# Kernel tuning notes

Measured on AMD Instinct MI355X. Metric: run time of the kernel, lower is better.

## Reference

```python
import jax, jax.numpy as jnp
import numpy as np

VOCAB, EMB, HID, TEMP = 10000, 256, 512, 0.5
EPS = 1e-20


def _lstm(x_seq, h0, c0, Wih, Whh, b):
    # x_seq: [T, B, E]; PyTorch gate order i, f, g, o
    def step(carry, x):
        h, c = carry
        gates = x @ Wih + h @ Whh + b
        i, f, g, o = jnp.split(gates, 4, axis=-1)
        c = jax.nn.sigmoid(f) * c + jax.nn.sigmoid(i) * jnp.tanh(g)
        h = jax.nn.sigmoid(o) * jnp.tanh(c)
        return (h, c), h
    (hT, cT), hs = jax.lax.scan(step, (h0, c0), x_seq)
    return hs, hT, cT


def setup_inputs() -> dict:
    key = jax.random.key(0)
    ks = jax.random.split(key, 16)
    B, T = 32, 128
    s = 0.02
    input_ids = jax.random.randint(ks[0], (B, T), 0, VOCAB, dtype=jnp.int32)
    mask = jax.random.randint(ks[1], (B, T), 0, 2, dtype=jnp.int32)
    U = jax.random.uniform(ks[2], (T, B, VOCAB), dtype=jnp.float32)
    gumbel_noise = -jnp.log(-jnp.log(U + EPS) + EPS)
    return {
        'input_ids': input_ids,
        'my_attention_mask': mask,
        'enc_embed': s * jax.random.normal(ks[3], (VOCAB, EMB), jnp.float32),
        'enc_Wih': s * jax.random.normal(ks[4], (EMB, 4 * HID), jnp.float32),
        'enc_Whh': s * jax.random.normal(ks[5], (HID, 4 * HID), jnp.float32),
        'enc_b': jnp.zeros((4 * HID,), jnp.float32),
        'dec_embed': s * jax.random.normal(ks[6], (VOCAB, EMB), jnp.float32),
        'dec_Wih': s * jax.random.normal(ks[7], (EMB, 4 * HID), jnp.float32),
        'dec_Whh': s * jax.random.normal(ks[8], (HID, 4 * HID), jnp.float32),
        'dec_b': jnp.zeros((4 * HID,), jnp.float32),
        'fc_W': s * jax.random.normal(ks[9], (HID, VOCAB), jnp.float32),
        'fc_b': jnp.zeros((VOCAB,), jnp.float32),
        'rand_init': jax.random.uniform(ks[10], (T, B, VOCAB), dtype=jnp.float32),
        'gumbel_noise': gumbel_noise,
    }


def reference(input_ids, my_attention_mask, enc_embed, enc_Wih, enc_Whh, enc_b,
              dec_embed, dec_Wih, dec_Whh, dec_b, fc_W, fc_b,
              rand_init, gumbel_noise):
    B, T = input_ids.shape
    mask = my_attention_mask                      # [B, T]
    tokens = input_ids.T                          # [T, B] (torch.t of view)

    h0 = jnp.zeros((B, HID), jnp.float32)
    # Encoder over full sequence
    _, hT, cT = _lstm(enc_embed[tokens], h0, h0, enc_Wih, enc_Whh, enc_b)
    # Decoder: teacher-forced on tokens[0:T-1] -> outputs for steps t=1..T-1
    hs, _, _ = _lstm(dec_embed[tokens[:-1]], hT, cT, dec_Wih, dec_Whh, dec_b)
    logits = hs @ fc_W + fc_b                     # [T-1, B, V]

    # Mask-driven compaction: outputs[sum(mask[j,:t]), j] = logits[t-1, j] where mask[j,t]==1
    excl = jnp.cumsum(mask, axis=1) - mask        # exclusive prefix sum [B, T]
    pos = excl[:, 1:]                             # [B, T-1]
    valid = mask[:, 1:] > 0
    pos_use = jnp.where(valid, pos, T)            # out-of-range -> dropped
    jj = jnp.broadcast_to(jnp.arange(B)[:, None], pos_use.shape)
    outputs = rand_init.at[pos_use, jj].set(jnp.swapaxes(logits, 0, 1), mode='drop')  # [T, B, V]

    # Hard gumbel-softmax with straight-through
    y = jax.nn.softmax((outputs + gumbel_noise) / TEMP, axis=-1)
    y_hard = jax.nn.one_hot(jnp.argmax(y, axis=-1), VOCAB, dtype=y.dtype)
    gs = jax.lax.stop_gradient(y_hard - y) + y    # [T, B, V]

    # Re-expand: masked positions take compacted gumbel rows, unmasked take token one-hots
    gathered = gs[excl, jnp.arange(B)[:, None]]   # [B, T, V]
    tok_oh = jax.nn.one_hot(input_ids, VOCAB, dtype=jnp.float32)
    onehots = jnp.where((mask > 0)[..., None], gathered, tok_oh)  # [B, T, V]
    return onehots.reshape(-1, VOCAB)             # dense form of the sparse inputs_embeds
```

## Files before the change

### kernel.cpp

```cpp
#include <hip/hip_runtime.h>
#include <hip/hip_bf16.h>
#include <math.h>

#define BB 32
#define TT 128
#define TD 127
#define EMB 256
#define HID 512
#define G4 2048
#define NV 10000
#define NB 64
#define NWK 192
#define GRID_UBER (NB + NWK)
#define UPB 8
#define NT_STEPS (TT + TD)

#define NJOB_DEC 512
#define NJOB_TR  313
#define NJOB_WN  20
#define NJOB_RM  4096
#define NJOBS (NJOB_DEC + NJOB_TR + NJOB_WN + NJOB_RM)

typedef __attribute__((ext_vector_type(8))) short short8v;
typedef __attribute__((ext_vector_type(4))) float f32x4;

__device__ __forceinline__ unsigned short bf16_rne(float x){
    unsigned int u = __float_as_uint(x);
    u += 0x7fffu + ((u >> 16) & 1u);
    return (unsigned short)(u >> 16);
}
__device__ __forceinline__ float bf16f(unsigned short h){
    return __uint_as_float(((unsigned int)h) << 16);
}

__global__ __launch_bounds__(256) void gemm_x(const int* __restrict__ ids,
        const float* __restrict__ embed, const float* __restrict__ W,
        const float* __restrict__ bias, float* __restrict__ X, int M)
{
    __shared__ float As[16][128];
    __shared__ float Bs[16][128];
    __shared__ int toks[128];
    const int tid = threadIdx.x;
    const int m0 = blockIdx.y * 128, n0 = blockIdx.x * 128;
    if (tid < 128) {
        int mr = m0 + tid, tk = 0;
        if (mr < M) { int t = mr >> 5, b = mr & 31; tk = ids[b*TT + t]; }
        toks[tid] = tk;
    }
    __syncthreads();
    float acc[8][8] = {};
    const int ty = tid >> 4, tx = tid & 15;
    for (int kt = 0; kt < EMB; kt += 16) {
        #pragma unroll
        for (int i = 0; i < 2; i++) {
            int idx = tid*2 + i;
            int row = idx >> 2, k4 = (idx & 3)*4;
            float4 a = *(const float4*)&embed[(size_t)toks[row]*EMB + kt + k4];
            As[k4+0][row] = a.x; As[k4+1][row] = a.y; As[k4+2][row] = a.z; As[k4+3][row] = a.w;
        }
        #pragma unroll
        for (int i = 0; i < 2; i++) {
            int idx = tid*2 + i;
            int kr = idx >> 5, c4 = (idx & 31)*4;
            *(float4*)&Bs[kr][c4] = *(const float4*)&W[(size_t)(kt+kr)*G4 + n0 + c4];
        }
        __syncthreads();
        #pragma unroll
        for (int k = 0; k < 16; k++) {
            float a8[8], b8[8];
            #pragma unroll
            for (int i = 0; i < 8; i++) a8[i] = As[k][ty*8+i];
            #pragma unroll
            for (int j = 0; j < 8; j++) b8[j] = Bs[k][tx*8+j];
            #pragma unroll
            for (int i = 0; i < 8; i++) {
                #pragma unroll
                for (int j = 0; j < 8; j++)
                    acc[i][j] = fmaf(a8[i], b8[j], acc[i][j]);
            }
        }
        __syncthreads();
    }
    #pragma unroll
    for (int i = 0; i < 8; i++) {
        int mr = m0 + ty*8 + i;
        if (mr < M) {
            int tt = mr >> 5, bb2 = mr & 31;
            #pragma unroll
            for (int j = 0; j < 8; j++) {
                int nc = n0 + tx*8 + j;
                X[((size_t)tt*G4 + nc)*BB + bb2] = acc[i][j] + bias[nc];
            }
        }
    }
}

__global__ __launch_bounds__(512) void lstm_persist(
        const float* __restrict__ Xenc, float* __restrict__ Xdec,
        const float* __restrict__ Whh_e, const float* __restrict__ Whh_d,
        unsigned int* __restrict__ h_pk,
        float* __restrict__ hs,
        int* __restrict__ flags,
        int* __restrict__ decdone,
        const int* __restrict__ ids, const float* __restrict__ dEmb,
        const float* __restrict__ dWih, const float* __restrict__ dB,
        const float* __restrict__ fcW, float* __restrict__ fcWt,
        const float* __restrict__ fcb, const int* __restrict__ mask,
        const float* __restrict__ gum, float* __restrict__ Mr,
        unsigned int* __restrict__ scal)
{
    __shared__ float smem[11392];
    const int tid = threadIdx.x;
    const int bid = blockIdx.x;

    if (bid >= NB) {
        const int wid = bid - NB;
        for (int job = wid; job < NJOBS; job += NWK) {
            if (job < NJOB_DEC) {
                const int my = job >> 4, nx = job & 15;
                const int m0 = my*128, n0 = nx*128;
                const int M = TD*BB;
                float* As = smem;
                float* Bs = smem + 2048;
                int* toks = (int*)(smem + 4096);
                if (tid < 128) {
                    int mr = m0 + tid, tk = 0;
                    if (mr < M) { int t = mr >> 5, b2 = mr & 31; tk = ids[b2*TT + t]; }
                    toks[tid] = tk;
                }
                __syncthreads();
                float acc[4][8] = {};
                const int ty = tid >> 4, tx = tid & 15;
                for (int kt = 0; kt < EMB; kt += 16) {
                    {
                        int row = tid >> 2, k4 = (tid & 3)*4;
                        float4 a = *(const float4*)&dEmb[(size_t)toks[row]*EMB + kt + k4];
                        As[(k4+0)*128+row] = a.x; As[(k4+1)*128+row] = a.y;
                        As[(k4+2)*128+row] = a.z; As[(k4+3)*128+row] = a.w;
                    }
                    {
                        int kr = tid >> 5, c4 = (tid & 31)*4;
                        *(float4*)&Bs[kr*128 + c4] =
                            *(const float4*)&dWih[(size_t)(kt+kr)*G4 + n0 + c4];
                    }
                    __syncthreads();
                    #pragma unroll
                    for (int k = 0; k < 16; k++) {
                        float a4[4], b8[8];
                        #pragma unroll
                        for (int i = 0; i < 4; i++) a4[i] = As[k*128 + ty*4+i];
                        #pragma unroll
                        for (int j = 0; j < 8; j++) b8[j] = Bs[k*128 + tx*8+j];
                        #pragma unroll
                        for (int i = 0; i < 4; i++) {
                            #pragma unroll
                            for (int j = 0; j < 8; j++)
                                acc[i][j] = fmaf(a4[i], b8[j], acc[i][j]);
                        }
                    }
                    __syncthreads();
                }
                #pragma unroll
                for (int i = 0; i < 4; i++) {
                    int mr = m0 + ty*4 + i;
                    if (mr < M) {
                        int t = mr >> 5, b2 = mr & 31;
                        #pragma unroll
                        for (int j = 0; j < 8; j++) {
                            int nc = n0 + tx*8 + j;
                            Xdec[((size_t)t*G4 + nc)*BB + b2] = acc[i][j] + dB[nc];
                        }
                    }
                }
                __syncthreads();
                if (tid == 0)
                    __hip_atomic_fetch_add(decdone, 1,
                        __ATOMIC_RELEASE, __HIP_MEMORY_SCOPE_AGENT);
            } else if (job < NJOB_DEC + NJOB_TR) {
                const int v0 = (job - NJOB_DEC)*32;
                float* tile = smem;
                for (int k0 = 0; k0 < HID; k0 += 16) {
                    {
                        int kk = tid >> 5, vv = tid & 31;
                        int v = v0 + vv;
                        tile[kk*33 + vv] = (v < NV) ? fcW[(size_t)(k0+kk)*NV + v] : 0.f;
                    }
                    __syncthreads();
                    {
                        int vy = tid >> 4, kx = tid & 15;
                        int v = v0 + vy;
                        if (v < NV) fcWt[(size_t)v*HID + k0 + kx] = tile[kx*33 + vy];
                    }
                    __syncthreads();
                }
            } else if (job < NJOB_DEC + NJOB_TR + NJOB_WN) {
                int v = (job - NJOB_DEC - NJOB_TR)*512 + tid;
                if (v < NV) {
                    float s = 0.f;
                    for (int k = 0; k < HID; k++) {
                        float x = fcW[(size_t)k*NV + v]; s = fmaf(x, x, s);
                    }
                    atomicMax(&scal[0], __float_as_uint(s));
                    atomicMax(&scal[1], __float_as_uint(fabsf(fcb[v])));
                }
            } else {
                const int row = job - NJOB_DEC - NJOB_TR - NJOB_WN;
                const int b = row >> 7, t = row & 127;
                const int mrow = mask[row];
                if (t != 0 && mrow != 0) {
                    int* wk = (int*)&smem[520];
                    int mi = (tid < TT) ? mask[b*TT + tid] : 0;
                    unsigned long long bal = __ballot(tid < t && mi != 0);
                    if ((tid & 63) == 0) wk[tid >> 6] = __popcll(bal);
                    __syncthreads();
                    int k = wk[0] + wk[1];
                    __syncthreads();
                    const float* g = gum + ((size_t)k*BB + b)*NV;
                    float m = -1e30f;
                    for (int v = tid; v < NV; v += 512) m = fmaxf(m, g[v]);
                    float* red = smem;
                    red[tid] = m; __syncthreads();
                    for (int s = 256; s; s >>= 1) {
                        if (tid < s) red[tid] = fmaxf(red[tid], red[tid+s]);
                        __syncthreads();
                    }
                    if (tid == 0) Mr[row] = red[0];
                    __syncthreads();
                }
            }
        }
        return;
    }

    float* partials = smem;
    float* xbuf     = smem + 9216;

    const int u0  = bid*UPB;
    const int w   = tid >> 6;
    const int l   = tid & 63;
    const int rl  = l & 15;
    const int kg  = (l >> 4) * 8;
    const int r4  = (l >> 4) * 4;
    const int gb  = tid >> 3, gul = tid & 7;

    short8v wH_n0k0, wH_n0k1, wH_n1k0, wH_n1k1;
    short8v wL_n0k0, wL_n0k1, wL_n1k0, wL_n1k1;

    #define BW(WH, WL, KB, CO) do { _Pragma("unroll") \
        for (int j = 0; j < 8; ++j) { \
            float wv2 = partials[((KB)+j)*32 + (CO) + rl]; \
            unsigned short htop = bf16_rne(wv2); \
            WH[j] = (short)htop; \
            WL[j] = (short)bf16_rne(wv2 - bf16f(htop)); \
        } } while(0)

    #define STAGE_BUILD(SRC) do { \
        for (int c = 0; c < 4; ++c) { \
            int k0 = c*128; \
            __syncthreads(); \
            for (int i = tid; i < 4096; i += 512) { \
                int kl = i >> 5, n = i & 31; \
                partials[kl*32 + n] = SRC[(size_t)(k0+kl)*G4 + (size_t)((n>>3)*512 + u0 + (n&7))]; \
            } \
            __syncthreads(); \
            if ((w >> 1) == c) { \
                int kb0 = w*64 - k0 + kg; \
                BW(wH_n0k0, wL_n0k0, kb0,      0); \
                BW(wH_n0k1, wL_n0k1, kb0 + 32, 0); \
                BW(wH_n1k0, wL_n1k0, kb0,     16); \
                BW(wH_n1k1, wL_n1k1, kb0 + 32,16); \
            } \
        } \
        __syncthreads(); } while(0)

    STAGE_BUILD(Whh_e);

    {
        for (int i = tid; i < 1024; i += 512) {
            int row2 = i & 31, n = i >> 5;
            xbuf[row2*33 + n] = Xenc[(size_t)((n>>3)*512 + u0 + (n&7))*32 + row2];
        }
        __syncthreads();
    }

    float c_reg = 0.f;

    #define MM6(ACC, AH0, AH1, AL0, AL1, WH0, WH1, WL0, WL1) do { \
        ACC = __builtin_amdgcn_mfma_f32_16x16x32_bf16(AH0, WH0, ACC, 0,0,0); \
        ACC = __builtin_amdgcn_mfma_f32_16x16x32_bf16(AH1, WH1, ACC, 0,0,0); \
        ACC = __builtin_amdgcn_mfma_f32_16x16x32_bf16(AL0, WH0, ACC, 0,0,0); \
        ACC = __builtin_amdgcn_mfma_f32_16x16x32_bf16(AL1, WH1, ACC, 0,0,0); \
        ACC = __builtin_amdgcn_mfma_f32_16x16x32_bf16(AH0, WL0, ACC, 0,0,0); \
        ACC = __builtin_amdgcn_mfma_f32_16x16x32_bf16(AH1, WL1, ACC, 0,0,0); \
    } while(0)

    for (int gstep = 0; gstep < NT_STEPS; ++gstep) {
        const bool enc = gstep < TT;
        const int t = enc ? gstep : gstep - TT;

        f32x4 acc00 = {0,0,0,0}, acc01 = {0,0,0,0}, acc10 = {0,0,0,0}, acc11 = {0,0,0,0};
        if (gstep > 0) {
            const unsigned int* hp = h_pk + (size_t)(gstep & 1)*16384;
            short8v aH_m0k0, aH_m0k1, aH_m1k0, aH_m1k1;
            short8v aL_m0k0, aL_m0k1, aL_m1k0, aL_m1k1;
            #define LOAD_A(AH, AL, MT, KS) do { \
                unsigned int pv[8]; \
                int kbase = w*64 + (KS)*32 + kg; \
                int brow = (MT)*16 + rl; \
                _Pragma("unroll") \
                for (int j = 0; j < 8; ++j) \
                    pv[j] = __hip_atomic_load(&hp[(kbase+j)*32 + brow], \
                                __ATOMIC_RELAXED, __HIP_MEMORY_SCOPE_AGENT); \
                _Pragma("unroll") \
                for (int j = 0; j < 8; ++j) { \
                    AH[j] = (short)(pv[j] & 0xffffu); \
                    AL[j] = (short)(pv[j] >> 16); \
                } } while(0)
            LOAD_A(aH_m0k0, aL_m0k0, 0, 0); LOAD_A(aH_m0k1, aL_m0k1, 0, 1);
            LOAD_A(aH_m1k0, aL_m1k0, 1, 0); LOAD_A(aH_m1k1, aL_m1k1, 1, 1);
            MM6(acc00, aH_m0k0, aH_m0k1, aL_m0k0, aL_m0k1, wH_n0k0, wH_n0k1, wL_n0k0, wL_n0k1);
            MM6(acc01, aH_m0k0, aH_m0k1, aL_m0k0, aL_m0k1, wH_n1k0, wH_n1k1, wL_n1k0, wL_n1k1);
            MM6(acc10, aH_m1k0, aH_m1k1, aL_m1k0, aL_m1k1, wH_n0k0, wH_n0k1, wL_n0k0, wL_n0k1);
            MM6(acc11, aH_m1k0, aH_m1k1, aL_m1k0, aL_m1k1, wH_n1k0, wH_n1k1, wL_n1k0, wL_n1k1);
        }
        #pragma unroll
        for (int j = 0; j < 4; ++j) {
            partials[(w*32 +      r4 + j)*36 +      rl] = acc00[j];
            partials[(w*32 +      r4 + j)*36 + 16 + rl] = acc01[j];
            partials[(w*32 + 16 + r4 + j)*36 +      rl] = acc10[j];
            partials[(w*32 + 16 + r4 + j)*36 + 16 + rl] = acc11[j];
        }
        __syncthreads();

        float hv = 0.f;
        if (tid < 256) {
            float pre[4];
            #pragma unroll
            for (int gg = 0; gg < 4; ++gg) {
                float s = xbuf[(gstep & 1)*1056 + gb*33 + gg*8 + gul];
                #pragma unroll
                for (int ww = 0; ww < 8; ++ww)
                    s += partials[(ww*32 + gb)*36 + gg*8 + gul];
                pre[gg] = s;
            }
            float iv = 1.f/(1.f + expf(-pre[0]));
            float fv = 1.f/(1.f + expf(-pre[1]));
            float gv = tanhf(pre[2]);
            float ov = 1.f/(1.f + expf(-pre[3]));
            c_reg = fmaf(fv, c_reg, iv*gv);
            hv = ov * tanhf(c_reg);
            unsigned short hh = bf16_rne(hv);
            unsigned short hl = bf16_rne(hv - bf16f(hh));
            unsigned int pk = (unsigned int)hh | ((unsigned int)hl << 16);
            __hip_atomic_store(&h_pk[(size_t)((gstep+1) & 1)*16384 + (u0+gul)*32 + gb],
                               pk, __ATOMIC_RELAXED, __HIP_MEMORY_SCOPE_AGENT);
        }
        __syncthreads();
        if (gstep < NT_STEPS - 1 && tid == 0)
            __hip_atomic_store(&flags[bid], gstep + 1,
                               __ATOMIC_RELAXED, __HIP_MEMORY_SCOPE_AGENT);
        if (!enc && tid < 256)
            hs[((size_t)t*BB + gb)*HID + u0 + gul] = hv;
        if (gstep == NT_STEPS - 1) break;

        if (gstep == TT - 1) STAGE_BUILD(Whh_d);

        {
            if (gstep + 1 == TT) {
                if (tid == 0) {
                    while (__hip_atomic_load(decdone, __ATOMIC_RELAXED,
                                             __HIP_MEMORY_SCOPE_AGENT) < NJOB_DEC)
                        __builtin_amdgcn_s_sleep(8);
                }
                __syncthreads();
                __builtin_amdgcn_fence(__ATOMIC_ACQUIRE, "agent");
            }
            int tn = gstep + 1 < TT ? gstep + 1 : gstep + 1 - TT;
            const float* Xt = (gstep + 1 < TT ? Xenc : (const float*)Xdec) + (size_t)tn*G4*BB;
            for (int i = tid; i < 1024; i += 512) {
                int row2 = i & 31, n = i >> 5;
                xbuf[((gstep+1) & 1)*1056 + row2*33 + n] =
                    Xt[(size_t)((n>>3)*512 + u0 + (n&7))*32 + row2];
            }
        }
        if (tid < NB) {
            while (__hip_atomic_load(&flags[tid], __ATOMIC_RELAXED,
                                     __HIP_MEMORY_SCOPE_AGENT) <= gstep) {}
        }
        __syncthreads();
        asm volatile("" ::: "memory");
    }
}

__global__ __launch_bounds__(256) void cand_write(
        const int* __restrict__ ids, const int* __restrict__ mask,
        const float* __restrict__ gum, const float* __restrict__ rinit,
        const float* __restrict__ hs, const float* __restrict__ Wt,
        const float* __restrict__ fcb, const float* __restrict__ Mr,
        const unsigned int* __restrict__ scal, float* __restrict__ out)
{
    const int row = blockIdx.x, b = row >> 7, t = row & 127;
    const int tid = threadIdx.x;
    __shared__ float red[256];
    __shared__ int idxr[256];
    __shared__ int list[256];
    __shared__ int wcnt[4];
    __shared__ int winsh;

    int win;
    if (mask[row] == 0) {
        win = ids[b*TT + t];
    } else if (t == 0) {
        const float* g  = gum   + (size_t)b*NV;
        const float* r0 = rinit + (size_t)b*NV;
        float bs = -1e30f; int bv = 0x7fffffff;
        for (int v = tid; v < NV; v += 256) {
            float sc = r0[v] + g[v];
            if (sc > bs) { bs = sc; bv = v; }
        }
        red[tid] = bs; idxr[tid] = bv; __syncthreads();
        for (int s = 128; s; s >>= 1) {
            if (tid < s) {
                if (red[tid+s] > red[tid] || (red[tid+s] == red[tid] && idxr[tid+s] < idxr[tid])) {
                    red[tid] = red[tid+s]; idxr[tid] = idxr[tid+s];
                }
            }
            __syncthreads();
        }
        win = idxr[0];
    } else {
        int mi = (tid < TT) ? mask[b*TT + tid] : 0;
        unsigned long long bal = __ballot(tid < t && mi != 0);
        if ((tid & 63) == 0) wcnt[tid >> 6] = __popcll(bal);
        __syncthreads();
        const int k = wcnt[0] + wcnt[1];
        __syncthreads();

        const float* g    = gum + ((size_t)k*BB + b)*NV;
        const float* hrow = hs + ((size_t)(t-1)*BB + b)*HID;
        float hn = 0.f;
        for (int k2 = tid; k2 < HID; k2 += 256) { float x = hrow[k2]; hn = fmaf(x, x, hn); }
        red[tid] = hn; __syncthreads();
        for (int s = 128; s; s >>= 1) {
            if (tid < s) red[tid] += red[tid+s];
            __syncthreads();
        }
        float bound = sqrtf(__uint_as_float(scal[0])) * sqrtf(red[0])
                    + __uint_as_float(scal[1]);
        float thr = Mr[row] - 2.0f*bound*1.05f - 1e-6f;
        __syncthreads();

        float curS = -1e30f; int curV = 0x7fffffff;
        int wv = tid >> 6, lane = tid & 63;
        for (int v0 = 0; v0 < NV; v0 += 256) {
            int v = v0 + tid;
            bool ok = (v < NV) && (g[v] >= thr);
            unsigned long long mb = __ballot(ok);
            if (lane == 0) wcnt[wv] = __popcll(mb);
            __syncthreads();
            int off = 0;
            #pragma unroll
            for (int w = 0; w < 4; w++) if (w < wv) off += wcnt[w];
            int tot = wcnt[0] + wcnt[1] + wcnt[2] + wcnt[3];
            if (ok) {
                int pos = off + __popcll(mb & ((1ull << lane) - 1ull));
                list[pos] = v;
            }
            __syncthreads();
            for (int ci = 0; ci < tot; ci++) {
                int vc = list[ci];
                float p = 0.f;
                for (int k2 = tid; k2 < HID; k2 += 256)
                    p = fmaf(hrow[k2], Wt[(size_t)vc*HID + k2], p);
                red[tid] = p; __syncthreads();
                for (int s = 128; s; s >>= 1) {
                    if (tid < s) red[tid] += red[tid+s];
                    __syncthreads();
                }
                if (tid == 0) {
                    float sc = (red[0] + fcb[vc]) + g[vc];
                    if (sc > curS || (sc == curS && vc < curV)) { curS = sc; curV = vc; }
                }
                __syncthreads();
            }
        }
        if (tid == 0) winsh = curV;
        __syncthreads();
        win = winsh;
    }

    float4* o = (float4*)(out + (size_t)row*NV);
    #pragma unroll
    for (int i = 0; i < 10; i++) {
        int idx = tid + i*256;
        if (idx < 2500) {
            int vb = idx*4;
            float4 val = {0.f, 0.f, 0.f, 0.f};
            if (win >= vb && win < vb+4) ((float*)&val)[win - vb] = 1.0f;
            o[idx] = val;
        }
    }
}

extern "C" void kernel_launch(void* const* d_in, const int* in_sizes, int n_in,
                              void* d_out, int out_size, void* d_ws, size_t ws_size,
                              hipStream_t stream)
{
    const int*   ids   = (const int*)d_in[0];
    const int*   mask  = (const int*)d_in[1];
    const float* eEmb  = (const float*)d_in[2];
    const float* eWih  = (const float*)d_in[3];
    const float* eWhh  = (const float*)d_in[4];
    const float* eB    = (const float*)d_in[5];
    const float* dEmb  = (const float*)d_in[6];
    const float* dWih  = (const float*)d_in[7];
    const float* dWhh  = (const float*)d_in[8];
    const float* dB    = (const float*)d_in[9];
    const float* fcW   = (const float*)d_in[10];
    const float* fcb   = (const float*)d_in[11];
    const float* rinit = (const float*)d_in[12];
    const float* gum   = (const float*)d_in[13];
    float* out = (float*)d_out;

    float* wsf = (float*)d_ws;
    size_t off = 0;
    float* Xenc = wsf + off; off += (size_t)TT*BB*G4;
    float* Xdec = wsf + off; off += (size_t)TD*BB*G4;
    unsigned int* h_pk = (unsigned int*)(wsf + off); off += 2*(size_t)BB*HID;
    float* hs   = wsf + off; off += (size_t)TD*BB*HID;
    float* fcWt = wsf + off; off += (size_t)NV*HID;
    float* Mr   = wsf + off; off += 4096;
    unsigned int* ctl = (unsigned int*)(wsf + off); off += 128;
    unsigned int* scal = ctl;
    int* flags   = (int*)(ctl + 8);
    int* decdone = (int*)(ctl + 72);

    hipMemsetAsync(ctl, 0, 128*sizeof(int), stream);

    dim3 gblk(16, 32);
    gemm_x<<<gblk, 256, 0, stream>>>(ids, eEmb, eWih, eB, Xenc, TT*BB);

    lstm_persist<<<GRID_UBER, 512, 0, stream>>>(Xenc, Xdec, eWhh, dWhh,
        h_pk, hs, flags, decdone,
        ids, dEmb, dWih, dB, fcW, fcWt, fcb, mask, gum, Mr, scal);

    cand_write<<<4096, 256, 0, stream>>>(ids, mask, gum, rinit, hs, fcWt, fcb,
                                         Mr, scal, out);
}
```

Before: 1.004 ms.

## Move one-hot output writes into persistent workers and precompute candidate lists

Worker blocks of the persistent LSTM kernel now write the full one-hot rows for unmasked and t==0 positions and zero-fill the masked rows. This overlaps the large output write with the latency-bound recurrence. The workers also record, per masked row, a short list of vocab entries whose gumbel noise lies within a fixed delta of the row maximum. cand_write then exits early for rows that are already written, and for masked rows it scores only that list when the norm bound allows, falling back to the full scan otherwise. In exchange, workspace use and worker job cost grow, and cand_write stores a single element into a row that was zeroed by an earlier kernel.

```diff
diff --git a/kernel.cpp b/kernel.cpp
--- a/kernel.cpp
+++ b/kernel.cpp
@@ -14,6 +14,8 @@
 #define GRID_UBER (NB + NWK)
 #define UPB 8
 #define NT_STEPS (TT + TD)
+#define CAND_CAP 16
+#define CAND_DELTA 1.0f
 
 #define NJOB_DEC 512
 #define NJOB_TR  313
@@ -106,8 +108,10 @@
         const float* __restrict__ dWih, const float* __restrict__ dB,
         const float* __restrict__ fcW, float* __restrict__ fcWt,
         const float* __restrict__ fcb, const int* __restrict__ mask,
-        const float* __restrict__ gum, float* __restrict__ Mr,
-        unsigned int* __restrict__ scal)
+        const float* __restrict__ gum, const float* __restrict__ rinit,
+        float* __restrict__ Mr, unsigned int* __restrict__ scal,
+        int* __restrict__ candCnt, int* __restrict__ candList,
+        float* __restrict__ outp)
 {
     __shared__ float smem[11392];
     const int tid = threadIdx.x;
@@ -207,14 +211,52 @@
                 const int row = job - NJOB_DEC - NJOB_TR - NJOB_WN;
                 const int b = row >> 7, t = row & 127;
                 const int mrow = mask[row];
-                if (t != 0 && mrow != 0) {
-                    int* wk = (int*)&smem[520];
+                float4* o = (float4*)(outp + (size_t)row*NV);
+                if (mrow == 0) {
+                    int win = ids[b*TT + t];
+                    for (int idx = tid; idx < 2500; idx += 512) {
+                        int vb = idx*4;
+                        float4 val = {0.f,0.f,0.f,0.f};
+                        if (win >= vb && win < vb+4) ((float*)&val)[win-vb] = 1.0f;
+                        o[idx] = val;
+                    }
+                } else if (t == 0) {
+                    const float* g  = gum   + (size_t)b*NV;
+                    const float* r0 = rinit + (size_t)b*NV;
+                    float bs = -1e30f; int bv = 0x7fffffff;
+                    for (int v = tid; v < NV; v += 512) {
+                        float sc = r0[v] + g[v];
+                        if (sc > bs || (sc == bs && v < bv)) { bs = sc; bv = v; }
+                    }
+                    float* red = smem;
+                    int* idxr = (int*)(smem + 512);
+                    red[tid] = bs; idxr[tid] = bv; __syncthreads();
+                    for (int s = 256; s; s >>= 1) {
+                        if (tid < s) {
+                            if (red[tid+s] > red[tid] ||
+                                (red[tid+s] == red[tid] && idxr[tid+s] < idxr[tid])) {
+                                red[tid] = red[tid+s]; idxr[tid] = idxr[tid+s];
+                            }
+                        }
+                        __syncthreads();
+                    }
+                    int win = idxr[0];
+                    __syncthreads();
+                    for (int idx = tid; idx < 2500; idx += 512) {
+                        int vb = idx*4;
+                        float4 val = {0.f,0.f,0.f,0.f};
+                        if (win >= vb && win < vb+4) ((float*)&val)[win-vb] = 1.0f;
+                        o[idx] = val;
+                    }
+                } else {
+                    int* wk   = (int*)&smem[1024];
+                    int* ccnt = (int*)&smem[1040];
                     int mi = (tid < TT) ? mask[b*TT + tid] : 0;
                     unsigned long long bal = __ballot(tid < t && mi != 0);
                     if ((tid & 63) == 0) wk[tid >> 6] = __popcll(bal);
-                    __syncthreads();
-                    int k = wk[0] + wk[1];
-                    __syncthreads();
+                    if (tid == 0) *ccnt = 0;
+                    __syncthreads();
+                    const int k = wk[0] + wk[1];
                     const float* g = gum + ((size_t)k*BB + b)*NV;
                     float m = -1e30f;
                     for (int v = tid; v < NV; v += 512) m = fmaxf(m, g[v]);
@@ -224,7 +266,18 @@
                         if (tid < s) red[tid] = fmaxf(red[tid], red[tid+s]);
                         __syncthreads();
                     }
-                    if (tid == 0) Mr[row] = red[0];
+                    const float Mv = red[0];
+                    const float thr0 = Mv - CAND_DELTA;
+                    for (int v = tid; v < NV; v += 512) {
+                        if (g[v] >= thr0) {
+                            int pos = atomicAdd(ccnt, 1);
+                            if (pos < CAND_CAP) candList[row*CAND_CAP + pos] = v;
+                        }
+                    }
+                    float4 z = {0.f,0.f,0.f,0.f};
+                    for (int idx = tid; idx < 2500; idx += 512) o[idx] = z;
+                    __syncthreads();
+                    if (tid == 0) { candCnt[row] = *ccnt; Mr[row] = Mv; }
                     __syncthreads();
                 }
             }
@@ -393,64 +446,63 @@
 }
 
 __global__ __launch_bounds__(256) void cand_write(
-        const int* __restrict__ ids, const int* __restrict__ mask,
-        const float* __restrict__ gum, const float* __restrict__ rinit,
+        const int* __restrict__ mask, const float* __restrict__ gum,
         const float* __restrict__ hs, const float* __restrict__ Wt,
         const float* __restrict__ fcb, const float* __restrict__ Mr,
-        const unsigned int* __restrict__ scal, float* __restrict__ out)
+        const unsigned int* __restrict__ scal,
+        const int* __restrict__ candCnt, const int* __restrict__ candList,
+        float* __restrict__ out)
 {
     const int row = blockIdx.x, b = row >> 7, t = row & 127;
+    if (t == 0 || mask[row] == 0) return;
     const int tid = threadIdx.x;
     __shared__ float red[256];
-    __shared__ int idxr[256];
     __shared__ int list[256];
     __shared__ int wcnt[4];
-    __shared__ int winsh;
-
-    int win;
-    if (mask[row] == 0) {
-        win = ids[b*TT + t];
-    } else if (t == 0) {
-        const float* g  = gum   + (size_t)b*NV;
-        const float* r0 = rinit + (size_t)b*NV;
-        float bs = -1e30f; int bv = 0x7fffffff;
-        for (int v = tid; v < NV; v += 256) {
-            float sc = r0[v] + g[v];
-            if (sc > bs) { bs = sc; bv = v; }
-        }
-        red[tid] = bs; idxr[tid] = bv; __syncthreads();
-        for (int s = 128; s; s >>= 1) {
-            if (tid < s) {
-                if (red[tid+s] > red[tid] || (red[tid+s] == red[tid] && idxr[tid+s] < idxr[tid])) {
-                    red[tid] = red[tid+s]; idxr[tid] = idxr[tid+s];
-                }
+
+    int mi = (tid < TT) ? mask[b*TT + tid] : 0;
+    unsigned long long bal = __ballot(tid < t && mi != 0);
+    if ((tid & 63) == 0) wcnt[tid >> 6] = __popcll(bal);
+    __syncthreads();
+    const int k = wcnt[0] + wcnt[1];
+    __syncthreads();
+
+    const float* g    = gum + ((size_t)k*BB + b)*NV;
+    const float* hrow = hs + ((size_t)(t-1)*BB + b)*HID;
+    float hn = 0.f;
+    for (int k2 = tid; k2 < HID; k2 += 256) { float x = hrow[k2]; hn = fmaf(x, x, hn); }
+    red[tid] = hn; __syncthreads();
+    for (int s = 128; s; s >>= 1) {
+        if (tid < s) red[tid] += red[tid+s];
+        __syncthreads();
+    }
+    const float Mv = Mr[row];
+    float bound = sqrtf(__uint_as_float(scal[0])) * sqrtf(red[0])
+                + __uint_as_float(scal[1]);
+    float thr = Mv - 2.0f*bound*1.05f - 1e-6f;
+    __syncthreads();
+
+    float curS = -1e30f; int curV = 0x7fffffff;
+    const int cnt = candCnt[row];
+
+    if (cnt <= CAND_CAP && thr >= Mv - CAND_DELTA) {
+        for (int ci = 0; ci < cnt; ci++) {
+            int vc = candList[row*CAND_CAP + ci];
+            float p = 0.f;
+            for (int k2 = tid; k2 < HID; k2 += 256)
+                p = fmaf(hrow[k2], Wt[(size_t)vc*HID + k2], p);
+            red[tid] = p; __syncthreads();
+            for (int s = 128; s; s >>= 1) {
+                if (tid < s) red[tid] += red[tid+s];
+                __syncthreads();
+            }
+            if (tid == 0) {
+                float sc = (red[0] + fcb[vc]) + g[vc];
+                if (sc > curS || (sc == curS && vc < curV)) { curS = sc; curV = vc; }
             }
             __syncthreads();
         }
-        win = idxr[0];
     } else {
-        int mi = (tid < TT) ? mask[b*TT + tid] : 0;
-        unsigned long long bal = __ballot(tid < t && mi != 0);
-        if ((tid & 63) == 0) wcnt[tid >> 6] = __popcll(bal);
-        __syncthreads();
-        const int k = wcnt[0] + wcnt[1];
-        __syncthreads();
-
-        const float* g    = gum + ((size_t)k*BB + b)*NV;
-        const float* hrow = hs + ((size_t)(t-1)*BB + b)*HID;
-        float hn = 0.f;
-        for (int k2 = tid; k2 < HID; k2 += 256) { float x = hrow[k2]; hn = fmaf(x, x, hn); }
-        red[tid] = hn; __syncthreads();
-        for (int s = 128; s; s >>= 1) {
-            if (tid < s) red[tid] += red[tid+s];
-            __syncthreads();
-        }
-        float bound = sqrtf(__uint_as_float(scal[0])) * sqrtf(red[0])
-                    + __uint_as_float(scal[1]);
-        float thr = Mr[row] - 2.0f*bound*1.05f - 1e-6f;
-        __syncthreads();
-
-        float curS = -1e30f; int curV = 0x7fffffff;
         int wv = tid >> 6, lane = tid & 63;
         for (int v0 = 0; v0 < NV; v0 += 256) {
             int v = v0 + tid;
@@ -484,22 +536,8 @@
                 __syncthreads();
             }
         }
-        if (tid == 0) winsh = curV;
-        __syncthreads();
-        win = winsh;
-    }
-
-    float4* o = (float4*)(out + (size_t)row*NV);
-    #pragma unroll
-    for (int i = 0; i < 10; i++) {
-        int idx = tid + i*256;
-        if (idx < 2500) {
-            int vb = idx*4;
-            float4 val = {0.f, 0.f, 0.f, 0.f};
-            if (win >= vb && win < vb+4) ((float*)&val)[win - vb] = 1.0f;
-            o[idx] = val;
-        }
-    }
+    }
+    if (tid == 0) out[(size_t)row*NV + curV] = 1.0f;
 }
 
 extern "C" void kernel_launch(void* const* d_in, const int* in_sizes, int n_in,
@@ -530,6 +568,8 @@
     float* hs   = wsf + off; off += (size_t)TD*BB*HID;
     float* fcWt = wsf + off; off += (size_t)NV*HID;
     float* Mr   = wsf + off; off += 4096;
+    int* candCnt  = (int*)(wsf + off); off += 4096;
+    int* candList = (int*)(wsf + off); off += 4096*CAND_CAP;
     unsigned int* ctl = (unsigned int*)(wsf + off); off += 128;
     unsigned int* scal = ctl;
     int* flags   = (int*)(ctl + 8);
@@ -542,8 +582,9 @@
 
     lstm_persist<<<GRID_UBER, 512, 0, stream>>>(Xenc, Xdec, eWhh, dWhh,
         h_pk, hs, flags, decdone,
-        ids, dEmb, dWih, dB, fcW, fcWt, fcb, mask, gum, Mr, scal);
-
-    cand_write<<<4096, 256, 0, stream>>>(ids, mask, gum, rinit, hs, fcWt, fcb,
-                                         Mr, scal, out);
+        ids, dEmb, dWih, dB, fcW, fcWt, fcb, mask, gum, rinit,
+        Mr, scal, candCnt, candList, out);
+
+    cand_write<<<4096, 256, 0, stream>>>(mask, gum, hs, fcWt, fcb,
+                                         Mr, scal, candCnt, candList, out);
 }
```

After: 967.9 us, median of 2. 3.6% less time.
